# Kernel optimization log

Measured on AMD Instinct MI355X. Metric: run time of the kernel, lower is better.

Reference implementation:

```python
import jax, jax.numpy as jnp
import numpy as np

NUM_TAGS = 128
NUM_FEATURES = 500000
B, T, F = 64, 512, 8


def setup_inputs() -> dict:
    key = jax.random.key(0)
    ks = jax.random.split(key, 6)
    feats = jax.random.randint(ks[0], (B, T, F), 0, NUM_FEATURES)
    tags = jax.random.randint(ks[1], (B, T), 0, NUM_TAGS)
    # original init: uniform(-0.01, 0.01)
    state_weights = jax.random.uniform(ks[2], (NUM_TAGS, NUM_FEATURES), minval=-0.01, maxval=0.01, dtype=jnp.float32)
    transitions = jax.random.uniform(ks[3], (NUM_TAGS, NUM_TAGS), minval=-0.01, maxval=0.01, dtype=jnp.float32)
    start_transitions = jax.random.uniform(ks[4], (NUM_TAGS,), minval=-0.01, maxval=0.01, dtype=jnp.float32)
    end_transitions = jax.random.uniform(ks[5], (NUM_TAGS,), minval=-0.01, maxval=0.01, dtype=jnp.float32)
    return dict(feats=feats, tags=tags, state_weights=state_weights,
                transitions=transitions, start_transitions=start_transitions,
                end_transitions=end_transitions)


def reference(feats, tags, state_weights, transitions, start_transitions, end_transitions):
    """Batched CRF negative log-likelihood per sentence: logZ - gold_score. Returns [B]."""
    # emissions[b,t,k] = sum_f state_weights[k, feats[b,t,f]]  (emissions_for_sentence)
    emissions = jnp.take(state_weights, feats, axis=1).sum(-1)   # [K,B,T]
    emissions = jnp.moveaxis(emissions, 0, -1)                    # [B,T,K]

    # log_partition: forward algorithm over T via scan
    alpha0 = start_transitions[None, :] + emissions[:, 0]         # [B,K]

    def step(alpha, em_t):
        # scores[b,i,j] = alpha[b,i] + transitions[i,j]
        scores = alpha[:, :, None] + transitions[None, :, :]
        return jax.nn.logsumexp(scores, axis=1) + em_t, None

    em_rest = jnp.moveaxis(emissions[:, 1:], 1, 0)                # [T-1,B,K]
    alphaT, _ = jax.lax.scan(step, alpha0, em_rest)
    log_z = jax.nn.logsumexp(alphaT + end_transitions[None, :], axis=1)   # [B]

    # gold_score, vectorized over batch
    em_gold = jnp.take_along_axis(emissions, tags[..., None], axis=2)[..., 0].sum(axis=1)  # [B]
    trans_gold = transitions[tags[:, :-1], tags[:, 1:]].sum(axis=1)                        # [B]
    gold = start_transitions[tags[:, 0]] + end_transitions[tags[:, -1]] + em_gold + trans_gold

    return log_z - gold
```

## Files before the change

kernel.cpp:

```cpp
#include <hip/hip_runtime.h>

#define NUM_TAGS 128
#define NUM_FEATS 500000
#define BB 64
#define TT 512
#define FF 8

#define SWT_BYTES 256000000ull
#define EM_BYTES  16777216ull
#define NEED_FULL (SWT_BYTES + EM_BYTES)

__global__ __launch_bounds__(256) void transpose_kernel(
    const float* __restrict__ sw, float* __restrict__ swT) {
  __shared__ float tile[32][129];
  const int f0 = blockIdx.x * 32;
  const int t = threadIdx.x;
  const int fi = t & 31, kb = t >> 5;
#pragma unroll
  for (int it = 0; it < 16; ++it) {
    int k = kb + it * 8;
    tile[fi][k] = sw[(size_t)k * NUM_FEATS + f0 + fi];
  }
  __syncthreads();
  const int k2 = t & 127, fo = t >> 7;
#pragma unroll
  for (int it = 0; it < 16; ++it) {
    int f2 = fo + it * 2;
    swT[(size_t)(f0 + f2) * NUM_TAGS + k2] = tile[f2][k2];
  }
}

__global__ __launch_bounds__(128) void gather_t_kernel(
    const int* __restrict__ feats, const float* __restrict__ swT,
    float* __restrict__ em_exp) {
  const int token = blockIdx.x;
  const int k = threadIdx.x;
  const int* f = feats + token * FF;
  float s = 0.f;
#pragma unroll
  for (int i = 0; i < FF; ++i) s += swT[(size_t)f[i] * NUM_TAGS + k];
  em_exp[(size_t)token * NUM_TAGS + k] = __expf(s);
}

__global__ __launch_bounds__(128) void gather_f_kernel(
    const int* __restrict__ feats, const float* __restrict__ sw,
    float* __restrict__ em_exp) {
  const int token = blockIdx.x;
  const int k = threadIdx.x;
  const int* f = feats + token * FF;
  const float* row = sw + (size_t)k * NUM_FEATS;
  float s = 0.f;
#pragma unroll
  for (int i = 0; i < FF; ++i) s += row[f[i]];
  em_exp[(size_t)token * NUM_TAGS + k] = __expf(s);
}

__global__ __launch_bounds__(512, 1) void fwd_kernel(
    const float* __restrict__ em_exp, const int* __restrict__ tags,
    const float* __restrict__ trans, const float* __restrict__ startT,
    const float* __restrict__ endT, float* __restrict__ out) {
  const int b = blockIdx.x;
  const int tid = threadIdx.x;
  const int q = tid >> 7, j = tid & 127;

  __shared__ __align__(16) float alpha[NUM_TAGS];
  __shared__ __align__(16) float partial[NUM_TAGS * 4];
  __shared__ float sred[16];

  float eT[32];
#pragma unroll
  for (int i = 0; i < 32; ++i)
    eT[i] = __expf(trans[(32 * q + i) * NUM_TAGS + j]);

  const float* embx = em_exp + (size_t)b * TT * NUM_TAGS;

  if (q == 0) alpha[j] = __expf(startT[j]) * embx[j];
  __syncthreads();

  float ev_next = embx[NUM_TAGS + j];
  for (int t = 1; t < TT; ++t) {
    float ev = ev_next;
    if (t + 1 < TT) ev_next = embx[(t + 1) * NUM_TAGS + j];

    const float4* a4 = (const float4*)alpha + q * 8;
    float acc = 0.f, acc2 = 0.f;
#pragma unroll
    for (int i = 0; i < 8; ++i) {
      float4 a = a4[i];
      acc  = fmaf(a.x, eT[4 * i + 0], acc);
      acc2 = fmaf(a.y, eT[4 * i + 1], acc2);
      acc  = fmaf(a.z, eT[4 * i + 2], acc);
      acc2 = fmaf(a.w, eT[4 * i + 3], acc2);
    }
    partial[j * 4 + q] = acc + acc2;
    __syncthreads();
    float4 p = *(const float4*)&partial[j * 4];
    if (q == 0) alpha[j] = (p.x + p.y + p.z + p.w) * ev * 0.0078125f;
    __syncthreads();
  }

  if (q == 0) {
    float val = alpha[j] * __expf(endT[j]);
#pragma unroll
    for (int off = 32; off > 0; off >>= 1) val += __shfl_down(val, off, 64);
    if ((j & 63) == 0) sred[j >> 6] = val;
  }

  const int* tb = tags + b * TT;
  const int t = tid;
  const int tg = tb[t];
  float g = __logf(embx[t * NUM_TAGS + tg]);
  if (t < TT - 1) g += trans[tg * NUM_TAGS + tb[t + 1]];
  if (t == 0) g += startT[tb[0]] + endT[tb[TT - 1]];
#pragma unroll
  for (int off = 32; off > 0; off >>= 1) g += __shfl_down(g, off, 64);
  if ((tid & 63) == 0) sred[8 + (tid >> 6)] = g;
  __syncthreads();

  if (tid == 0) {
    float logz = __logf(sred[0] + sred[1]) + 511.0f * 7.0f * 0.69314718055994531f;
    float gs = 0.f;
#pragma unroll
    for (int i = 0; i < 8; ++i) gs += sred[8 + i];
    out[b] = logz - gs;
  }
}

extern "C" void kernel_launch(void* const* d_in, const int* in_sizes, int n_in,
                              void* d_out, int out_size, void* d_ws, size_t ws_size,
                              hipStream_t stream) {
  const int* feats = (const int*)d_in[0];
  const int* tags = (const int*)d_in[1];
  const float* sw = (const float*)d_in[2];
  const float* trans = (const float*)d_in[3];
  const float* startT = (const float*)d_in[4];
  const float* endT = (const float*)d_in[5];
  float* out = (float*)d_out;

  if (ws_size >= NEED_FULL) {
    float* swT = (float*)d_ws;
    float* em_exp = (float*)((char*)d_ws + SWT_BYTES);
    transpose_kernel<<<NUM_FEATS / 32, 256, 0, stream>>>(sw, swT);
    gather_t_kernel<<<BB * TT, 128, 0, stream>>>(feats, swT, em_exp);
    fwd_kernel<<<BB, 512, 0, stream>>>(em_exp, tags, trans, startT, endT, out);
  } else {
    float* em_exp = (float*)d_ws;
    gather_f_kernel<<<BB * TT, 128, 0, stream>>>(feats, sw, em_exp);
    fwd_kernel<<<BB, 512, 0, stream>>>(em_exp, tags, trans, startT, endT, out);
  }
}
```

Measured before the change: 565.3 us.

## Fuse emission gather into forward recursion with prefetched feature loads

Removes the separate gather kernel and its emission buffer; each 128-thread block now gathers its token emissions on the fly from the transposed weight table. Loads are prefetched four timesteps ahead through rotating register buffers, and feature and tag indices are staged in shared memory. The recursion uses one thread per tag with a full 128-wide dot product held as packed float2 registers, ping-ponging alpha buffers so each step needs one barrier. This trades parallelism in the serial recursion (128 threads per block instead of 512) and risks gather latency sitting on the critical path, in exchange for dropping a kernel launch and the emission round trip through global memory.

```diff
diff --git a/kernel.cpp b/kernel.cpp
--- a/kernel.cpp
+++ b/kernel.cpp
@@ -7,8 +7,8 @@
 #define FF 8
 
 #define SWT_BYTES 256000000ull
-#define EM_BYTES  16777216ull
-#define NEED_FULL (SWT_BYTES + EM_BYTES)
+
+typedef float f2 __attribute__((ext_vector_type(2)));
 
 __global__ __launch_bounds__(256) void transpose_kernel(
     const float* __restrict__ sw, float* __restrict__ swT) {
@@ -25,104 +25,139 @@
   const int k2 = t & 127, fo = t >> 7;
 #pragma unroll
   for (int it = 0; it < 16; ++it) {
-    int f2 = fo + it * 2;
-    swT[(size_t)(f0 + f2) * NUM_TAGS + k2] = tile[f2][k2];
+    int f2i = fo + it * 2;
+    swT[(size_t)(f0 + f2i) * NUM_TAGS + k2] = tile[f2i][k2];
   }
 }
 
-__global__ __launch_bounds__(128) void gather_t_kernel(
-    const int* __restrict__ feats, const float* __restrict__ swT,
-    float* __restrict__ em_exp) {
-  const int token = blockIdx.x;
-  const int k = threadIdx.x;
-  const int* f = feats + token * FF;
-  float s = 0.f;
-#pragma unroll
-  for (int i = 0; i < FF; ++i) s += swT[(size_t)f[i] * NUM_TAGS + k];
-  em_exp[(size_t)token * NUM_TAGS + k] = __expf(s);
+template <bool TR>
+__device__ __forceinline__ void loadf(float (&buf)[8], const int* sfeats, int t,
+                                      const float* __restrict__ swx, int j) {
+  const int4 fa = ((const int4*)sfeats)[t * 2];
+  const int4 fb = ((const int4*)sfeats)[t * 2 + 1];
+  if (TR) {
+    buf[0] = swx[(size_t)fa.x * NUM_TAGS + j];
+    buf[1] = swx[(size_t)fa.y * NUM_TAGS + j];
+    buf[2] = swx[(size_t)fa.z * NUM_TAGS + j];
+    buf[3] = swx[(size_t)fa.w * NUM_TAGS + j];
+    buf[4] = swx[(size_t)fb.x * NUM_TAGS + j];
+    buf[5] = swx[(size_t)fb.y * NUM_TAGS + j];
+    buf[6] = swx[(size_t)fb.z * NUM_TAGS + j];
+    buf[7] = swx[(size_t)fb.w * NUM_TAGS + j];
+  } else {
+    const float* row = swx + (size_t)j * NUM_FEATS;
+    buf[0] = row[fa.x]; buf[1] = row[fa.y]; buf[2] = row[fa.z]; buf[3] = row[fa.w];
+    buf[4] = row[fb.x]; buf[5] = row[fb.y]; buf[6] = row[fb.z]; buf[7] = row[fb.w];
+  }
 }
 
-__global__ __launch_bounds__(128) void gather_f_kernel(
-    const int* __restrict__ feats, const float* __restrict__ sw,
-    float* __restrict__ em_exp) {
-  const int token = blockIdx.x;
-  const int k = threadIdx.x;
-  const int* f = feats + token * FF;
-  const float* row = sw + (size_t)k * NUM_FEATS;
-  float s = 0.f;
+template <bool TR>
+__device__ __forceinline__ void stepf(float (&buf)[8], const int* sfeats,
+                                      const int* stags, int t,
+                                      const float* __restrict__ swx, int j,
+                                      const float* alf_src, float* alf_dst,
+                                      const f2 (&eT2)[64], float& gold_em) {
+  float s = ((buf[0] + buf[1]) + (buf[2] + buf[3])) +
+            ((buf[4] + buf[5]) + (buf[6] + buf[7]));
+  int tn = t + 4; if (tn > TT - 1) tn = TT - 1;
+  loadf<TR>(buf, sfeats, tn, swx, j);
+  float ev = __expf(s);
+  if (j == stags[t]) gold_em += s;
+  f2 acc0 = {0.f, 0.f}, acc1 = {0.f, 0.f}, acc2 = {0.f, 0.f}, acc3 = {0.f, 0.f};
+  const float4* a4 = (const float4*)alf_src;
 #pragma unroll
-  for (int i = 0; i < FF; ++i) s += row[f[i]];
-  em_exp[(size_t)token * NUM_TAGS + k] = __expf(s);
+  for (int i = 0; i < 16; ++i) {
+    float4 a = a4[2 * i];
+    float4 b = a4[2 * i + 1];
+    acc0 += (f2){a.x, a.y} * eT2[4 * i + 0];
+    acc1 += (f2){a.z, a.w} * eT2[4 * i + 1];
+    acc2 += (f2){b.x, b.y} * eT2[4 * i + 2];
+    acc3 += (f2){b.z, b.w} * eT2[4 * i + 3];
+  }
+  f2 sA = acc0 + acc2, sB = acc1 + acc3;
+  float dot = (sA.x + sA.y) + (sB.x + sB.y);
+  alf_dst[j] = dot * ev * 0.0078125f;
+  __syncthreads();
 }
 
-__global__ __launch_bounds__(512, 1) void fwd_kernel(
-    const float* __restrict__ em_exp, const int* __restrict__ tags,
-    const float* __restrict__ trans, const float* __restrict__ startT,
-    const float* __restrict__ endT, float* __restrict__ out) {
+template <bool TR>
+__global__ __launch_bounds__(128) void fwd_fused_kernel(
+    const int* __restrict__ feats, const int* __restrict__ tags,
+    const float* __restrict__ swx, const float* __restrict__ trans,
+    const float* __restrict__ startT, const float* __restrict__ endT,
+    float* __restrict__ out) {
   const int b = blockIdx.x;
-  const int tid = threadIdx.x;
-  const int q = tid >> 7, j = tid & 127;
+  const int j = threadIdx.x;
 
-  __shared__ __align__(16) float alpha[NUM_TAGS];
-  __shared__ __align__(16) float partial[NUM_TAGS * 4];
-  __shared__ float sred[16];
+  __shared__ __align__(16) float alf[2][NUM_TAGS];
+  __shared__ __align__(16) int sfeats[TT * FF];
+  __shared__ __align__(16) int stags[TT];
+  __shared__ float sred[4];
 
-  float eT[32];
+  const int4* gF = (const int4*)(feats + (size_t)b * TT * FF);
+  int4* sF4 = (int4*)sfeats;
 #pragma unroll
-  for (int i = 0; i < 32; ++i)
-    eT[i] = __expf(trans[(32 * q + i) * NUM_TAGS + j]);
+  for (int p = 0; p < 8; ++p) sF4[j + 128 * p] = gF[j + 128 * p];
+  ((int4*)stags)[j] = ((const int4*)(tags + (size_t)b * TT))[j];
 
-  const float* embx = em_exp + (size_t)b * TT * NUM_TAGS;
-
-  if (q == 0) alpha[j] = __expf(startT[j]) * embx[j];
+  f2 eT2[64];
+#pragma unroll
+  for (int m = 0; m < 64; ++m) {
+    eT2[m].x = __expf(trans[(2 * m) * NUM_TAGS + j]);
+    eT2[m].y = __expf(trans[(2 * m + 1) * NUM_TAGS + j]);
+  }
   __syncthreads();
 
-  float ev_next = embx[NUM_TAGS + j];
-  for (int t = 1; t < TT; ++t) {
-    float ev = ev_next;
-    if (t + 1 < TT) ev_next = embx[(t + 1) * NUM_TAGS + j];
+  float bA[8], bB[8], bC[8], bD[8];
+  float gold_em = 0.f;
 
-    const float4* a4 = (const float4*)alpha + q * 8;
-    float acc = 0.f, acc2 = 0.f;
-#pragma unroll
-    for (int i = 0; i < 8; ++i) {
-      float4 a = a4[i];
-      acc  = fmaf(a.x, eT[4 * i + 0], acc);
-      acc2 = fmaf(a.y, eT[4 * i + 1], acc2);
-      acc  = fmaf(a.z, eT[4 * i + 2], acc);
-      acc2 = fmaf(a.w, eT[4 * i + 3], acc2);
-    }
-    partial[j * 4 + q] = acc + acc2;
-    __syncthreads();
-    float4 p = *(const float4*)&partial[j * 4];
-    if (q == 0) alpha[j] = (p.x + p.y + p.z + p.w) * ev * 0.0078125f;
+  loadf<TR>(bA, sfeats, 0, swx, j);
+  loadf<TR>(bB, sfeats, 1, swx, j);
+  loadf<TR>(bC, sfeats, 2, swx, j);
+  loadf<TR>(bD, sfeats, 3, swx, j);
+
+  {
+    float s = ((bA[0] + bA[1]) + (bA[2] + bA[3])) +
+              ((bA[4] + bA[5]) + (bA[6] + bA[7]));
+    loadf<TR>(bA, sfeats, 4, swx, j);
+    float ev = __expf(s);
+    if (j == stags[0]) gold_em += s;
+    alf[0][j] = __expf(startT[j]) * ev;
     __syncthreads();
   }
 
-  if (q == 0) {
-    float val = alpha[j] * __expf(endT[j]);
+  int cur = 0;
+  for (int t = 1; t + 6 < TT; t += 4) {
+    stepf<TR>(bB, sfeats, stags, t + 0, swx, j, alf[cur], alf[cur ^ 1], eT2, gold_em); cur ^= 1;
+    stepf<TR>(bC, sfeats, stags, t + 1, swx, j, alf[cur], alf[cur ^ 1], eT2, gold_em); cur ^= 1;
+    stepf<TR>(bD, sfeats, stags, t + 2, swx, j, alf[cur], alf[cur ^ 1], eT2, gold_em); cur ^= 1;
+    stepf<TR>(bA, sfeats, stags, t + 3, swx, j, alf[cur], alf[cur ^ 1], eT2, gold_em); cur ^= 1;
+  }
+  stepf<TR>(bB, sfeats, stags, 509, swx, j, alf[cur], alf[cur ^ 1], eT2, gold_em); cur ^= 1;
+  stepf<TR>(bC, sfeats, stags, 510, swx, j, alf[cur], alf[cur ^ 1], eT2, gold_em); cur ^= 1;
+  stepf<TR>(bD, sfeats, stags, 511, swx, j, alf[cur], alf[cur ^ 1], eT2, gold_em); cur ^= 1;
+
+  float val = alf[cur][j] * __expf(endT[j]);
 #pragma unroll
-    for (int off = 32; off > 0; off >>= 1) val += __shfl_down(val, off, 64);
-    if ((j & 63) == 0) sred[j >> 6] = val;
+  for (int off = 32; off > 0; off >>= 1) val += __shfl_down(val, off, 64);
+  if ((j & 63) == 0) sred[j >> 6] = val;
+
+  float g = gold_em;
+#pragma unroll
+  for (int p = 0; p < 4; ++p) {
+    int t = j + 128 * p;
+    int tg = stags[t];
+    if (t < TT - 1) g += trans[tg * NUM_TAGS + stags[t + 1]];
   }
-
-  const int* tb = tags + b * TT;
-  const int t = tid;
-  const int tg = tb[t];
-  float g = __logf(embx[t * NUM_TAGS + tg]);
-  if (t < TT - 1) g += trans[tg * NUM_TAGS + tb[t + 1]];
-  if (t == 0) g += startT[tb[0]] + endT[tb[TT - 1]];
+  if (j == 0) g += startT[stags[0]] + endT[stags[TT - 1]];
 #pragma unroll
   for (int off = 32; off > 0; off >>= 1) g += __shfl_down(g, off, 64);
-  if ((tid & 63) == 0) sred[8 + (tid >> 6)] = g;
+  if ((j & 63) == 0) sred[2 + (j >> 6)] = g;
   __syncthreads();
 
-  if (tid == 0) {
+  if (j == 0) {
     float logz = __logf(sred[0] + sred[1]) + 511.0f * 7.0f * 0.69314718055994531f;
-    float gs = 0.f;
-#pragma unroll
-    for (int i = 0; i < 8; ++i) gs += sred[8 + i];
-    out[b] = logz - gs;
+    out[b] = logz - (sred[2] + sred[3]);
   }
 }
 
@@ -137,15 +172,11 @@
   const float* endT = (const float*)d_in[5];
   float* out = (float*)d_out;
 
-  if (ws_size >= NEED_FULL) {
+  if (ws_size >= SWT_BYTES) {
     float* swT = (float*)d_ws;
-    float* em_exp = (float*)((char*)d_ws + SWT_BYTES);
     transpose_kernel<<<NUM_FEATS / 32, 256, 0, stream>>>(sw, swT);
-    gather_t_kernel<<<BB * TT, 128, 0, stream>>>(feats, swT, em_exp);
-    fwd_kernel<<<BB, 512, 0, stream>>>(em_exp, tags, trans, startT, endT, out);
+    fwd_fused_kernel<true><<<BB, 128, 0, stream>>>(feats, tags, swT, trans, startT, endT, out);
   } else {
-    float* em_exp = (float*)d_ws;
-    gather_f_kernel<<<BB * TT, 128, 0, stream>>>(feats, sw, em_exp);
-    fwd_kernel<<<BB, 512, 0, stream>>>(em_exp, tags, trans, startT, endT, out);
+    fwd_fused_kernel<false><<<BB, 128, 0, stream>>>(feats, tags, sw, trans, startT, endT, out);
   }
 }
```

Measured after the change: 650.5 us. 15.1% more time.

## Use shuffle reduction and double-buffered alpha to halve barriers in CRF forward

Applied to the files above, without the earlier changes.

Remaps threads so the four partial sums for each tag sit in adjacent lanes and are combined with xor shuffles instead of a shared-memory partial array. Alpha is double-buffered in padded LDS, which leaves one lightweight barrier per time step instead of two. The change also uses packed 2-wide float multiply-adds and prefetches emissions four steps ahead. The serial 511-step recurrence is latency-bound, so cutting barriers per step should shorten the critical path, at the cost of more complex indexing and an unrolled tail.

```diff
diff --git a/kernel.cpp b/kernel.cpp
--- a/kernel.cpp
+++ b/kernel.cpp
@@ -9,6 +9,16 @@
 #define SWT_BYTES 256000000ull
 #define EM_BYTES  16777216ull
 #define NEED_FULL (SWT_BYTES + EM_BYTES)
+
+typedef float f2 __attribute__((ext_vector_type(2)));
+
+#define AP(j) ((((j) >> 5) * 36) + ((j) & 31))
+
+__device__ __forceinline__ void barrier_lds() {
+  asm volatile("s_waitcnt lgkmcnt(0)" ::: "memory");
+  __builtin_amdgcn_s_barrier();
+  __builtin_amdgcn_sched_barrier(0);
+}
 
 __global__ __launch_bounds__(256) void transpose_kernel(
     const float* __restrict__ sw, float* __restrict__ swT) {
@@ -25,8 +35,8 @@
   const int k2 = t & 127, fo = t >> 7;
 #pragma unroll
   for (int it = 0; it < 16; ++it) {
-    int f2 = fo + it * 2;
-    swT[(size_t)(f0 + f2) * NUM_TAGS + k2] = tile[f2][k2];
+    int f2i = fo + it * 2;
+    swT[(size_t)(f0 + f2i) * NUM_TAGS + k2] = tile[f2i][k2];
   }
 }
 
@@ -55,55 +65,70 @@
   em_exp[(size_t)token * NUM_TAGS + k] = __expf(s);
 }
 
+__device__ __forceinline__ void stepv(float& evreg, int t,
+                                      const float* __restrict__ embx,
+                                      int j, int q, const float* alf_src,
+                                      float* alf_dst, const f2 (&eTv)[16]) {
+  float ev = evreg;
+  int tp = t + 4; if (tp > TT - 1) tp = TT - 1;
+  evreg = embx[tp * NUM_TAGS + j];
+  const float4* a4 = (const float4*)(alf_src + q * 36);
+  f2 acc0 = {0.f, 0.f}, acc1 = {0.f, 0.f};
+#pragma unroll
+  for (int i = 0; i < 8; ++i) {
+    float4 a = a4[i];
+    acc0 += (f2){a.x, a.y} * eTv[2 * i];
+    acc1 += (f2){a.z, a.w} * eTv[2 * i + 1];
+  }
+  float r = (acc0.x + acc0.y) + (acc1.x + acc1.y);
+  r += __shfl_xor(r, 1, 64);
+  r += __shfl_xor(r, 2, 64);
+  if (q == 0) alf_dst[AP(j)] = r * ev * 0.0078125f;
+  barrier_lds();
+}
+
 __global__ __launch_bounds__(512, 1) void fwd_kernel(
     const float* __restrict__ em_exp, const int* __restrict__ tags,
     const float* __restrict__ trans, const float* __restrict__ startT,
     const float* __restrict__ endT, float* __restrict__ out) {
   const int b = blockIdx.x;
   const int tid = threadIdx.x;
-  const int q = tid >> 7, j = tid & 127;
+  const int j = tid >> 2, q = tid & 3;
 
-  __shared__ __align__(16) float alpha[NUM_TAGS];
-  __shared__ __align__(16) float partial[NUM_TAGS * 4];
+  __shared__ __align__(16) float alf[2][144];
   __shared__ float sred[16];
 
-  float eT[32];
+  f2 eTv[16];
 #pragma unroll
-  for (int i = 0; i < 32; ++i)
-    eT[i] = __expf(trans[(32 * q + i) * NUM_TAGS + j]);
+  for (int i = 0; i < 16; ++i) {
+    eTv[i].x = __expf(trans[(32 * q + 2 * i) * NUM_TAGS + j]);
+    eTv[i].y = __expf(trans[(32 * q + 2 * i + 1) * NUM_TAGS + j]);
+  }
 
   const float* embx = em_exp + (size_t)b * TT * NUM_TAGS;
 
-  if (q == 0) alpha[j] = __expf(startT[j]) * embx[j];
+  if (q == 0) alf[0][AP(j)] = __expf(startT[j]) * embx[j];
+
+  float evA = embx[1 * NUM_TAGS + j], evB = embx[2 * NUM_TAGS + j],
+        evC = embx[3 * NUM_TAGS + j], evD = embx[4 * NUM_TAGS + j];
   __syncthreads();
 
-  float ev_next = embx[NUM_TAGS + j];
-  for (int t = 1; t < TT; ++t) {
-    float ev = ev_next;
-    if (t + 1 < TT) ev_next = embx[(t + 1) * NUM_TAGS + j];
+  int cur = 0;
+  for (int t = 1; t + 3 < TT; t += 4) {
+    stepv(evA, t + 0, embx, j, q, alf[cur], alf[cur ^ 1], eTv); cur ^= 1;
+    stepv(evB, t + 1, embx, j, q, alf[cur], alf[cur ^ 1], eTv); cur ^= 1;
+    stepv(evC, t + 2, embx, j, q, alf[cur], alf[cur ^ 1], eTv); cur ^= 1;
+    stepv(evD, t + 3, embx, j, q, alf[cur], alf[cur ^ 1], eTv); cur ^= 1;
+  }
+  stepv(evA, 509, embx, j, q, alf[cur], alf[cur ^ 1], eTv); cur ^= 1;
+  stepv(evB, 510, embx, j, q, alf[cur], alf[cur ^ 1], eTv); cur ^= 1;
+  stepv(evC, 511, embx, j, q, alf[cur], alf[cur ^ 1], eTv); cur ^= 1;
 
-    const float4* a4 = (const float4*)alpha + q * 8;
-    float acc = 0.f, acc2 = 0.f;
-#pragma unroll
-    for (int i = 0; i < 8; ++i) {
-      float4 a = a4[i];
-      acc  = fmaf(a.x, eT[4 * i + 0], acc);
-      acc2 = fmaf(a.y, eT[4 * i + 1], acc2);
-      acc  = fmaf(a.z, eT[4 * i + 2], acc);
-      acc2 = fmaf(a.w, eT[4 * i + 3], acc2);
-    }
-    partial[j * 4 + q] = acc + acc2;
-    __syncthreads();
-    float4 p = *(const float4*)&partial[j * 4];
-    if (q == 0) alpha[j] = (p.x + p.y + p.z + p.w) * ev * 0.0078125f;
-    __syncthreads();
-  }
-
-  if (q == 0) {
-    float val = alpha[j] * __expf(endT[j]);
+  if (tid < 128) {
+    float val = alf[cur][AP(tid)] * __expf(endT[tid]);
 #pragma unroll
     for (int off = 32; off > 0; off >>= 1) val += __shfl_down(val, off, 64);
-    if ((j & 63) == 0) sred[j >> 6] = val;
+    if ((tid & 63) == 0) sred[tid >> 6] = val;
   }
 
   const int* tb = tags + b * TT;
```

After: 565.4 us. Within noise of the previous version (+0.0%).
